# Kernel tuning notes

Hardware: AMD Instinct MI355X
Metric: run time of the kernel (lower is better)

Reference implementation:

```python
import jax, jax.numpy as jnp
import numpy as np

GRID = 2
SPAN = 2.0
EMBED = 64
HIDDEN = 128
PRED_LEN = 12
N = 1024
T = 8
SCENE_SIZE = 64


def _social_pool(ht, pos, scene, active):
    """ht: [N,H], pos: [N,2], scene: [N] int, active: [N] bool -> [N, GRID*GRID, H].
    Vectorized equivalent of the per-scene scatter_add pooling: pairwise mask over
    same-scene, active, within-area, non-self pairs; bin neighbor hidden states."""
    n = ht.shape[0]
    half = SPAN / 2.0
    eps = 0.01
    rel = pos[None, :, :] - pos[:, None, :]  # rel[i,j] = pos_j - pos_i
    within = ((rel[..., 0] < half - eps) & (rel[..., 0] > -half + eps)
              & (rel[..., 1] < half - eps) & (rel[..., 1] > -half + eps))
    pair = (within & (~jnp.eye(n, dtype=bool))
            & (scene[:, None] == scene[None, :])
            & active[:, None] & active[None, :])
    cell = SPAN / GRID
    gidx = jnp.floor((rel + half) / cell).astype(jnp.int32)
    gid = jnp.clip(gidx[..., 0] * GRID + gidx[..., 1], 0, GRID * GRID - 1)
    onehot = jax.nn.one_hot(gid, GRID * GRID, dtype=ht.dtype) * pair[..., None].astype(ht.dtype)
    # pooled[i,g,h] = sum_j onehot[i,j,g] * ht[j,h]
    return jnp.einsum('ijg,jh->igh', onehot, ht)


def _lstm_step(x, h, c, Wih, Whh, bih, bhh):
    z = x @ Wih.T + bih + h @ Whh.T + bhh
    i, f, g, o = jnp.split(z, 4, axis=-1)
    c_new = jax.nn.sigmoid(f) * c + jax.nn.sigmoid(i) * jnp.tanh(g)
    h_new = jax.nn.sigmoid(o) * jnp.tanh(c_new)
    return h_new, c_new


def setup_inputs() -> dict:
    key = jax.random.key(0)
    ks = jax.random.split(key, 16)
    past_traj = jax.random.uniform(ks[0], (N, T, 2), dtype=jnp.float32) * 8.0
    past_traj_rel = jax.random.normal(ks[1], (N, T, 2), dtype=jnp.float32)
    past_traj_timestamp_mask = jnp.ones((N, T), dtype=jnp.int32)
    is_predictable = jnp.ones((N, 1), dtype=jnp.int32)
    same_scene_mask = (jnp.arange(N, dtype=jnp.int32) // SCENE_SIZE).reshape(N, 1)

    def lin(k, fan_out, fan_in):
        b = 1.0 / np.sqrt(fan_in)
        return jax.random.uniform(k, (fan_out, fan_in), jnp.float32, -b, b)

    pos_W = lin(ks[2], EMBED, 2)
    pos_b = jnp.zeros((EMBED,), jnp.float32)
    soc_W = lin(ks[3], EMBED, GRID * GRID * HIDDEN)
    soc_b = jnp.zeros((EMBED,), jnp.float32)
    Wih = lin(ks[4], 4 * HIDDEN, 2 * EMBED)
    Whh = lin(ks[5], 4 * HIDDEN, HIDDEN)
    bih = jnp.zeros((4 * HIDDEN,), jnp.float32)
    bhh = jnp.zeros((4 * HIDDEN,), jnp.float32)
    h0 = jax.random.normal(ks[6], (HIDDEN,), jnp.float32) * 0.1
    c0 = jax.random.normal(ks[7], (HIDDEN,), jnp.float32) * 0.1
    pred_W = lin(ks[8], 5, HIDDEN)
    pred_b = jnp.zeros((5,), jnp.float32)
    return {
        'past_traj': past_traj, 'past_traj_rel': past_traj_rel,
        'past_traj_timestamp_mask': past_traj_timestamp_mask,
        'is_predictable': is_predictable, 'same_scene_mask': same_scene_mask,
        'pos_W': pos_W, 'pos_b': pos_b, 'soc_W': soc_W, 'soc_b': soc_b,
        'Wih': Wih, 'Whh': Whh, 'bih': bih, 'bhh': bhh,
        'h0': h0, 'c0': c0, 'pred_W': pred_W, 'pred_b': pred_b,
    }


def reference(past_traj, past_traj_rel, past_traj_timestamp_mask, is_predictable,
              same_scene_mask, pos_W, pos_b, soc_W, soc_b, Wih, Whh, bih, bhh,
              h0, c0, pred_W, pred_b):
    n = past_traj.shape[0]
    scene = same_scene_mask[:, 0]
    ht = jnp.broadcast_to(h0[None, :], (n, HIDDEN))
    ct = jnp.broadcast_to(c0[None, :], (n, HIDDEN))

    def obs_step(carry, inp):
        ht, ct = carry
        point, rel, m = inp  # [N,2], [N,2], [N]
        active = m == 1
        pooled = _social_pool(ht, point, scene, active)  # [N,G^2,H]
        et = jax.nn.relu(rel @ pos_W.T + pos_b)
        at = jax.nn.relu(pooled.reshape(n, -1) @ soc_W.T + soc_b)
        x = jnp.concatenate([et, at], axis=-1)
        h_new, c_new = _lstm_step(x, ht, ct, Wih, Whh, bih, bhh)
        ht = jnp.where(active[:, None], h_new, ht)
        ct = jnp.where(active[:, None], c_new, ct)
        return (ht, ct), None

    obs_inp = (jnp.moveaxis(past_traj, 1, 0), jnp.moveaxis(past_traj_rel, 1, 0),
               jnp.moveaxis(past_traj_timestamp_mask, 1, 0))
    (ht, ct), _ = jax.lax.scan(obs_step, (ht, ct), obs_inp)

    pred_active = past_traj_timestamp_mask[:, -1] == 1
    pos0 = past_traj[:, -1, :]

    def pred_step(carry, _):
        ht, ct, pos = carry
        out = ht @ pred_W.T + pred_b  # [N,5]
        rel = out[:, :2]
        pos = pos + rel
        pooled = _social_pool(ht, pos, scene, pred_active)
        et = jax.nn.relu(rel @ pos_W.T + pos_b)
        at = jax.nn.relu(pooled.reshape(n, -1) @ soc_W.T + soc_b)
        x = jnp.concatenate([et, at], axis=-1)
        h_new, c_new = _lstm_step(x, ht, ct, Wih, Whh, bih, bhh)
        ht = jnp.where(pred_active[:, None], h_new, ht)
        ct = jnp.where(pred_active[:, None], c_new, ct)
        return (ht, ct, pos), (out, pos)

    (_, _, _), (outs, trajs) = jax.lax.scan(pred_step, (ht, ct, pos0), None, length=PRED_LEN)
    pred_out_all = jnp.where(pred_active[:, None, None], jnp.moveaxis(outs, 0, 1), 0.0)
    pred_traj_all = jnp.where(pred_active[:, None, None], jnp.moveaxis(trajs, 0, 1), 0.0)
    # is_predictable is all-ones in this setup, so the final boolean filter is identity
    return pred_out_all, pred_traj_all
```

## Files before the change

kernel.cpp:

```cpp
#include <hip/hip_runtime.h>

#define NAGENT 64
#define HID    128
#define TOBS   8
#define PREDL  12
#define NTHR   1024
#define XH     136
#define PP     264
#define SPP    268

typedef __attribute__((ext_vector_type(8))) short bf16x8;
typedef __attribute__((ext_vector_type(4))) short bf16x4;
typedef __attribute__((ext_vector_type(4))) float f32x4;
typedef __attribute__((ext_vector_type(4))) int   i32x4;
typedef __attribute__((ext_vector_type(2))) unsigned int u32x2;

__device__ __forceinline__ unsigned short f2bf(float f) {
    unsigned int x = __float_as_uint(f);
    unsigned int r = (x + 0x7fffu + ((x >> 16) & 1u)) >> 16;
    return (unsigned short)r;
}
__device__ __forceinline__ float bf2f(unsigned short u) {
    return __uint_as_float(((unsigned int)u) << 16);
}
__device__ __forceinline__ float sigmf(float x) {
    return __builtin_amdgcn_rcpf(1.0f + __expf(-x));
}
__device__ __forceinline__ float tanhf_fast(float x) {
    x = fminf(fmaxf(x, -15.0f), 15.0f);
    float e = __expf(2.0f * x);
    return (e - 1.0f) * __builtin_amdgcn_rcpf(e + 1.0f);
}
__device__ __forceinline__ float sel4(float a0, float a1, float a2, float a3, int k) {
    float lo = (k & 1) ? a1 : a0;
    float hi = (k & 1) ? a3 : a2;
    return (k & 2) ? hi : lo;
}

__global__ void prep_weights(const float* __restrict__ Wih, const float* __restrict__ Whh,
                             const float* __restrict__ socW, const float* __restrict__ predW,
                             unsigned short* __restrict__ wd, unsigned short* __restrict__ wb,
                             unsigned short* __restrict__ wp) {
    int idx = blockIdx.x * 256 + threadIdx.x;
    if (idx < 131072) {
        int e = idx & 7, l = (idx >> 3) & 63, t = idx >> 9;
        int kt = t & 7, nt = t >> 3;
        int k = kt * 32 + ((l >> 4) << 3) + e;
        int n = nt * 16 + (l & 15);
        int d = n >> 2, g = n & 3;
        int row = g * 128 + d;
        float v = (k < 128) ? Wih[row * 128 + k] : Whh[row * 128 + (k - 128)];
        wd[idx] = f2bf(v);
    } else if (idx < 163840) {
        int i2 = idx - 131072;
        int e = i2 & 7, l = (i2 >> 3) & 63, t = i2 >> 9;
        int kt = t & 3, nt = t >> 2;
        int k = kt * 32 + ((l >> 4) << 3) + e;
        int r = nt * 16 + (l & 15);
        int eo = r >> 2, g = r & 3;
        wb[i2] = f2bf(socW[eo * 512 + g * 128 + k]);
    } else if (idx < 167936) {
        int i3 = idx - 163840;
        int e = i3 & 7, l = (i3 >> 3) & 63, f = i3 >> 9;
        int kt = f & 3, half = f >> 2;
        int k = kt * 32 + ((l >> 4) << 3) + e;
        int n = l & 15;
        float v = (n < 5) ? predW[n * 128 + k] : 0.0f;
        unsigned short hi = f2bf(v);
        wp[i3] = half ? f2bf(v - bf2f(hi)) : hi;
    }
}

__global__ __launch_bounds__(NTHR) void social_lstm_mfma(
    const float* __restrict__ past_traj, const float* __restrict__ past_traj_rel,
    const int* __restrict__ ts_mask, const int* __restrict__ scene_in,
    const float* __restrict__ pos_W, const float* __restrict__ pos_b,
    const float* __restrict__ soc_b,
    const float* __restrict__ bih, const float* __restrict__ bhh,
    const float* __restrict__ h0, const float* __restrict__ c0,
    const float* __restrict__ pred_b,
    const unsigned short* __restrict__ wd, const unsigned short* __restrict__ wb,
    const unsigned short* __restrict__ wp,
    float* __restrict__ out)
{
    __shared__ __align__(16) unsigned short sh_X[NAGENT][XH];
    __shared__ __align__(16) unsigned short sh_H[2][NAGENT][XH];
    __shared__ __align__(16) unsigned short sh_P[NAGENT][PP];
    __shared__ __align__(16) unsigned short sh_S[NAGENT][SPP];
    __shared__ float sh_px[2][NAGENT], sh_py[2][NAGENT];
    __shared__ float sh_rx[2][NAGENT], sh_ry[2][NAGENT];
    __shared__ __align__(16) int sh_act[2][NAGENT];
    __shared__ int sh_scene[NAGENT];

    const int tid  = threadIdx.x;
    const int lane = tid & 63;
    const int wv   = __builtin_amdgcn_readfirstlane(tid >> 6);
    const int gbase = blockIdx.x * NAGENT;
    const int c16 = lane & 15;
    const int q4  = lane >> 4;
    const int go  = c16 & 3;
    const int dq  = c16 >> 2;

    float bs[2], c_st[4][2];
    int dimv[2];
    #pragma unroll
    for (int s = 0; s < 2; ++s) {
        const int n = (2 * wv + s) * 16 + c16;
        const int d = n >> 2, g = n & 3;
        bs[s] = bih[g * 128 + d] + bhh[g * 128 + d];
        dimv[s] = (2 * wv + s) * 4 + dq;
        #pragma unroll
        for (int mj = 0; mj < 4; ++mj) c_st[mj][s] = c0[dimv[s]];
    }
    for (int p = tid; p < NAGENT * HID; p += NTHR) {
        int a = p >> 7, d = p & 127;
        sh_H[0][a][d] = f2bf(h0[d]);
    }
    if (tid < NAGENT) {
        const int ig = gbase + tid;
        sh_scene[tid] = scene_in[ig];
        sh_px[0][tid] = past_traj[(ig * TOBS + 0) * 2 + 0];
        sh_py[0][tid] = past_traj[(ig * TOBS + 0) * 2 + 1];
        sh_rx[0][tid] = past_traj_rel[(ig * TOBS + 0) * 2 + 0];
        sh_ry[0][tid] = past_traj_rel[(ig * TOBS + 0) * 2 + 1];
        sh_act[0][tid] = (ts_mask[ig * TOBS + 0] == 1) ? 1 : 0;
    }
    __syncthreads();

    const bf16x8* wdp = (const bf16x8*)wd + (2 * wv * 8) * 64 + lane;
    const bf16x8* wbp = (const bf16x8*)wb + (wv * 4) * 64 + lane;

    for (int step = 0; step < TOBS + PREDL; ++step) {
        const int pb = step & 1;
        const int hb = step & 1;
        const int ab = (step < TOBS) ? pb : 1;

        if (step >= TOBS) {
            if (wv < 4) {
                const bf16x8* wpv = (const bf16x8*)wp;
                f32x4 pa = (f32x4){0.f, 0.f, 0.f, 0.f};
                #pragma unroll
                for (int kt = 0; kt < 4; ++kt) {
                    const bf16x8 a = *(const bf16x8*)&sh_H[hb][wv * 16 + c16][kt * 32 + q4 * 8];
                    pa = __builtin_amdgcn_mfma_f32_16x16x32_bf16(a, wpv[kt * 64 + lane], pa, 0, 0, 0);
                    pa = __builtin_amdgcn_mfma_f32_16x16x32_bf16(a, wpv[(4 + kt) * 64 + lane], pa, 0, 0, 0);
                }
                if (c16 < 5) {
                    const float pbias = pred_b[c16];
                    const int p = step - TOBS;
                    const int pprev = (step - 1) & 1;
                    #pragma unroll
                    for (int rr = 0; rr < 4; ++rr) {
                        const int a = wv * 16 + q4 * 4 + rr;
                        const float o = pa[rr] + pbias;
                        const float m = sh_act[1][a] ? 1.0f : 0.0f;
                        const int ig = gbase + a;
                        out[(ig * PREDL + p) * 5 + c16] = m * o;
                        if (c16 == 0) {
                            const float px = sh_px[pprev][a] + o;
                            sh_px[pb][a] = px; sh_rx[pb][a] = o;
                            out[61440 + (ig * PREDL + p) * 2 + 0] = m * px;
                        }
                        if (c16 == 1) {
                            const float py = sh_py[pprev][a] + o;
                            sh_py[pb][a] = py; sh_ry[pb][a] = o;
                            out[61440 + (ig * PREDL + p) * 2 + 1] = m * py;
                        }
                    }
                }
            }
            __syncthreads();
        }

        #pragma unroll
        for (int it = 0; it < 4; ++it) {
            const int p = it * NTHR + tid;
            const int i = p >> 6, j = p & 63;
            const float dx = sh_px[pb][j] - sh_px[pb][i];
            const float dy = sh_py[pb][j] - sh_py[pb][i];
            const bool within = (dx < 0.99f) & (dx > -0.99f) & (dy < 0.99f) & (dy > -0.99f);
            const bool pair = within && (i != j) && (sh_scene[i] == sh_scene[j])
                              && sh_act[ab][i] && sh_act[ab][j];
            const int gid = ((dx >= 0.f) ? 2 : 0) + ((dy >= 0.f) ? 1 : 0);
            unsigned int w0 = 0, w1 = 0;
            if (pair) {
                if (gid == 0) w0 = 0x3f80u;
                else if (gid == 1) w0 = 0x3f800000u;
                else if (gid == 2) w1 = 0x3f80u;
                else w1 = 0x3f800000u;
            }
            u32x2 w; w[0] = w0; w[1] = w1;
            *(u32x2*)&sh_P[i][j * 4] = w;
        }
        {
            const float rx = sh_rx[pb][lane], ry = sh_ry[pb][lane];
            const int e0 = wv * 4;
            #pragma unroll
            for (int u = 0; u < 4; ++u) {
                const int e = e0 + u;
                sh_X[lane][e] = f2bf(fmaxf(pos_b[e] + rx * pos_W[e * 2] + ry * pos_W[e * 2 + 1], 0.f));
            }
        }
        {
            f32x4 acc2[4];
            #pragma unroll
            for (int mj = 0; mj < 4; ++mj) acc2[mj] = (f32x4){0.f, 0.f, 0.f, 0.f};
            #pragma unroll
            for (int kt = 0; kt < 4; ++kt) {
                const bf16x8 b = wbp[kt * 64];
                #pragma unroll
                for (int mj = 0; mj < 4; ++mj) {
                    const bf16x8 a = *(const bf16x8*)&sh_H[hb][mj * 16 + c16][kt * 32 + q4 * 8];
                    acc2[mj] = __builtin_amdgcn_mfma_f32_16x16x32_bf16(a, b, acc2[mj], 0, 0, 0);
                }
            }
            const int rcol = wv * 16 + c16;
            #pragma unroll
            for (int mj = 0; mj < 4; ++mj)
                #pragma unroll
                for (int rr = 0; rr < 4; ++rr)
                    sh_S[mj * 16 + q4 * 4 + rr][rcol] = f2bf(acc2[mj][rr]);
        }
        __syncthreads();

        {
            const int mt = wv & 3, nt = wv >> 2;
            const int cb = 4 * (nt * 16 + c16);
            f32x4 cac = (f32x4){0.f, 0.f, 0.f, 0.f};
            #pragma unroll
            for (int kt = 0; kt < 8; ++kt) {
                const bf16x8 a = *(const bf16x8*)&sh_P[mt * 16 + c16][kt * 32 + q4 * 8];
                const int j0 = kt * 8 + q4 * 2;
                const bf16x4 lo = *(const bf16x4*)&sh_S[j0][cb];
                const bf16x4 hi = *(const bf16x4*)&sh_S[j0 + 1][cb];
                const bf16x8 b = __builtin_shufflevector(lo, hi, 0, 1, 2, 3, 4, 5, 6, 7);
                cac = __builtin_amdgcn_mfma_f32_16x16x32_bf16(a, b, cac, 0, 0, 0);
            }
            const int e = nt * 16 + c16;
            const float sb = soc_b[e];
            #pragma unroll
            for (int rr = 0; rr < 4; ++rr)
                sh_X[mt * 16 + q4 * 4 + rr][64 + e] = f2bf(fmaxf(cac[rr] + sb, 0.f));
        }
        __syncthreads();

        {
            f32x4 acc[4][2];
            #pragma unroll
            for (int mj = 0; mj < 4; ++mj) {
                acc[mj][0] = (f32x4){0.f, 0.f, 0.f, 0.f};
                acc[mj][1] = (f32x4){0.f, 0.f, 0.f, 0.f};
            }
            #pragma unroll 2
            for (int kt = 0; kt < 8; ++kt) {
                const bf16x8 b0 = wdp[kt * 64];
                const bf16x8 b1 = wdp[kt * 64 + 512];
                #pragma unroll
                for (int mj = 0; mj < 4; ++mj) {
                    const bf16x8 a = (kt < 4)
                        ? *(const bf16x8*)&sh_X[mj * 16 + c16][kt * 32 + q4 * 8]
                        : *(const bf16x8*)&sh_H[hb][mj * 16 + c16][(kt - 4) * 32 + q4 * 8];
                    acc[mj][0] = __builtin_amdgcn_mfma_f32_16x16x32_bf16(a, b0, acc[mj][0], 0, 0, 0);
                    acc[mj][1] = __builtin_amdgcn_mfma_f32_16x16x32_bf16(a, b1, acc[mj][1], 0, 0, 0);
                }
            }
            #pragma unroll
            for (int mj = 0; mj < 4; ++mj) {
                const int a = mj * 16 + q4 * 4 + go;
                const bool act = sh_act[ab][a] != 0;
                #pragma unroll
                for (int s = 0; s < 2; ++s) {
                    const float z0 = acc[mj][s][0] + bs[s];
                    const float z1 = acc[mj][s][1] + bs[s];
                    const float z2 = acc[mj][s][2] + bs[s];
                    const float z3 = acc[mj][s][3] + bs[s];
                    const float s0 = sel4(z0, z1, z2, z3, go);
                    const float s1 = sel4(z0, z1, z2, z3, go ^ 1);
                    const float s2 = sel4(z0, z1, z2, z3, go ^ 2);
                    const float s3 = sel4(z0, z1, z2, z3, go ^ 3);
                    const float t1 = __shfl_xor(s1, 1, 64);
                    const float t2 = __shfl_xor(s2, 2, 64);
                    const float t3 = __shfl_xor(s3, 3, 64);
                    const float zi = sel4(s0, t1, t2, t3, go);
                    const float zf = sel4(s0, t1, t2, t3, go ^ 1);
                    const float zg = sel4(s0, t1, t2, t3, go ^ 2);
                    const float zo = sel4(s0, t1, t2, t3, go ^ 3);
                    const float cold = c_st[mj][s];
                    const float cn = sigmf(zf) * cold + sigmf(zi) * tanhf_fast(zg);
                    const float hn = sigmf(zo) * tanhf_fast(cn);
                    c_st[mj][s] = act ? cn : cold;
                    const float hold = bf2f(sh_H[hb][a][dimv[s]]);
                    sh_H[hb ^ 1][a][dimv[s]] = f2bf(act ? hn : hold);
                }
            }
        }
        if (step + 1 < TOBS && tid < NAGENT) {
            const int ig = gbase + tid;
            const int np = (step + 1) & 1;
            sh_px[np][tid] = past_traj[(ig * TOBS + step + 1) * 2 + 0];
            sh_py[np][tid] = past_traj[(ig * TOBS + step + 1) * 2 + 1];
            sh_rx[np][tid] = past_traj_rel[(ig * TOBS + step + 1) * 2 + 0];
            sh_ry[np][tid] = past_traj_rel[(ig * TOBS + step + 1) * 2 + 1];
            sh_act[np][tid] = (ts_mask[ig * TOBS + step + 1] == 1) ? 1 : 0;
        }
        __syncthreads();
    }
}

extern "C" void kernel_launch(void* const* d_in, const int* in_sizes, int n_in,
                              void* d_out, int out_size, void* d_ws, size_t ws_size,
                              hipStream_t stream) {
    (void)in_sizes; (void)n_in; (void)out_size; (void)ws_size;
    unsigned short* wd = (unsigned short*)d_ws;
    unsigned short* wb = wd + 131072;
    unsigned short* wp = wb + 32768;
    prep_weights<<<656, 256, 0, stream>>>(
        (const float*)d_in[9], (const float*)d_in[10],
        (const float*)d_in[7], (const float*)d_in[15], wd, wb, wp);
    social_lstm_mfma<<<16, NTHR, 0, stream>>>(
        (const float*)d_in[0],
        (const float*)d_in[1],
        (const int*)  d_in[2],
        (const int*)  d_in[4],
        (const float*)d_in[5],
        (const float*)d_in[6],
        (const float*)d_in[8],
        (const float*)d_in[11],
        (const float*)d_in[12],
        (const float*)d_in[13],
        (const float*)d_in[14],
        (const float*)d_in[16],
        wd, wb, wp,
        (float*)d_out);
}
```

Measured before the change: 299.0 us.

## Retile LSTM gate GEMM so each lane owns all four gates per dimension

Reorders the packed LSTM weights to the natural gate-major row order. Each wave now computes all four gates (i,f,g,o) for 16 hidden dims across 2 agent tiles, instead of interleaved gate columns. This removes the cross-lane shuffles and select chains in the cell update and keeps h in registers rather than rereading the old h from LDS. The social GEMM is retiled to 2x2 tiles per wave with the same goal of reusing A and B operands, which raises per-wave B-fragment global loads and register pressure.

```diff
diff --git a/kernel.cpp b/kernel.cpp
--- a/kernel.cpp
+++ b/kernel.cpp
@@ -30,11 +30,6 @@
     x = fminf(fmaxf(x, -15.0f), 15.0f);
     float e = __expf(2.0f * x);
     return (e - 1.0f) * __builtin_amdgcn_rcpf(e + 1.0f);
-}
-__device__ __forceinline__ float sel4(float a0, float a1, float a2, float a3, int k) {
-    float lo = (k & 1) ? a1 : a0;
-    float hi = (k & 1) ? a3 : a2;
-    return (k & 2) ? hi : lo;
 }
 
 __global__ void prep_weights(const float* __restrict__ Wih, const float* __restrict__ Whh,
@@ -47,9 +42,7 @@
         int kt = t & 7, nt = t >> 3;
         int k = kt * 32 + ((l >> 4) << 3) + e;
         int n = nt * 16 + (l & 15);
-        int d = n >> 2, g = n & 3;
-        int row = g * 128 + d;
-        float v = (k < 128) ? Wih[row * 128 + k] : Whh[row * 128 + (k - 128)];
+        float v = (k < 128) ? Wih[n * 128 + k] : Whh[n * 128 + (k - 128)];
         wd[idx] = f2bf(v);
     } else if (idx < 163840) {
         int i2 = idx - 131072;
@@ -98,19 +91,22 @@
     const int gbase = blockIdx.x * NAGENT;
     const int c16 = lane & 15;
     const int q4  = lane >> 4;
-    const int go  = c16 & 3;
-    const int dq  = c16 >> 2;
-
-    float bs[2], c_st[4][2];
-    int dimv[2];
-    #pragma unroll
-    for (int s = 0; s < 2; ++s) {
-        const int n = (2 * wv + s) * 16 + c16;
-        const int d = n >> 2, g = n & 3;
-        bs[s] = bih[g * 128 + d] + bhh[g * 128 + d];
-        dimv[s] = (2 * wv + s) * 4 + dq;
+
+    const int sub8 = wv & 7;
+    const int mjg  = wv >> 3;
+    const int dim  = sub8 * 16 + c16;
+
+    const float bs0 = bih[0 * 128 + dim] + bhh[0 * 128 + dim];
+    const float bs1 = bih[1 * 128 + dim] + bhh[1 * 128 + dim];
+    const float bs2 = bih[2 * 128 + dim] + bhh[2 * 128 + dim];
+    const float bs3 = bih[3 * 128 + dim] + bhh[3 * 128 + dim];
+    float c_st[2][4], h_rg[2][4];
+    {
+        const float cz = c0[dim], hz = h0[dim];
         #pragma unroll
-        for (int mj = 0; mj < 4; ++mj) c_st[mj][s] = c0[dimv[s]];
+        for (int m = 0; m < 2; ++m)
+            #pragma unroll
+            for (int r = 0; r < 4; ++r) { c_st[m][r] = cz; h_rg[m][r] = hz; }
     }
     for (int p = tid; p < NAGENT * HID; p += NTHR) {
         int a = p >> 7, d = p & 127;
@@ -127,8 +123,8 @@
     }
     __syncthreads();
 
-    const bf16x8* wdp = (const bf16x8*)wd + (2 * wv * 8) * 64 + lane;
-    const bf16x8* wbp = (const bf16x8*)wb + (wv * 4) * 64 + lane;
+    const bf16x8* wdv = (const bf16x8*)wd;
+    const bf16x8* wbv = (const bf16x8*)wb;
 
     for (int step = 0; step < TOBS + PREDL; ++step) {
         const int pb = step & 1;
@@ -202,24 +198,29 @@
             }
         }
         {
-            f32x4 acc2[4];
-            #pragma unroll
-            for (int mj = 0; mj < 4; ++mj) acc2[mj] = (f32x4){0.f, 0.f, 0.f, 0.f};
+            f32x4 bac[2][2];
+            bac[0][0] = (f32x4){0,0,0,0}; bac[0][1] = (f32x4){0,0,0,0};
+            bac[1][0] = (f32x4){0,0,0,0}; bac[1][1] = (f32x4){0,0,0,0};
             #pragma unroll
             for (int kt = 0; kt < 4; ++kt) {
-                const bf16x8 b = wbp[kt * 64];
-                #pragma unroll
-                for (int mj = 0; mj < 4; ++mj) {
-                    const bf16x8 a = *(const bf16x8*)&sh_H[hb][mj * 16 + c16][kt * 32 + q4 * 8];
-                    acc2[mj] = __builtin_amdgcn_mfma_f32_16x16x32_bf16(a, b, acc2[mj], 0, 0, 0);
-                }
-            }
-            const int rcol = wv * 16 + c16;
-            #pragma unroll
-            for (int mj = 0; mj < 4; ++mj)
-                #pragma unroll
-                for (int rr = 0; rr < 4; ++rr)
-                    sh_S[mj * 16 + q4 * 4 + rr][rcol] = f2bf(acc2[mj][rr]);
+                const bf16x8 a0 = *(const bf16x8*)&sh_H[hb][(2 * mjg + 0) * 16 + c16][kt * 32 + q4 * 8];
+                const bf16x8 a1 = *(const bf16x8*)&sh_H[hb][(2 * mjg + 1) * 16 + c16][kt * 32 + q4 * 8];
+                const bf16x8 b0 = wbv[((2 * sub8 + 0) * 4 + kt) * 64 + lane];
+                const bf16x8 b1 = wbv[((2 * sub8 + 1) * 4 + kt) * 64 + lane];
+                bac[0][0] = __builtin_amdgcn_mfma_f32_16x16x32_bf16(a0, b0, bac[0][0], 0, 0, 0);
+                bac[0][1] = __builtin_amdgcn_mfma_f32_16x16x32_bf16(a0, b1, bac[0][1], 0, 0, 0);
+                bac[1][0] = __builtin_amdgcn_mfma_f32_16x16x32_bf16(a1, b0, bac[1][0], 0, 0, 0);
+                bac[1][1] = __builtin_amdgcn_mfma_f32_16x16x32_bf16(a1, b1, bac[1][1], 0, 0, 0);
+            }
+            #pragma unroll
+            for (int mjl = 0; mjl < 2; ++mjl)
+                #pragma unroll
+                for (int s = 0; s < 2; ++s) {
+                    const int rcol = (2 * sub8 + s) * 16 + c16;
+                    #pragma unroll
+                    for (int rr = 0; rr < 4; ++rr)
+                        sh_S[(2 * mjg + mjl) * 16 + q4 * 4 + rr][rcol] = f2bf(bac[mjl][s][rr]);
+                }
         }
         __syncthreads();
 
@@ -245,52 +246,42 @@
         __syncthreads();
 
         {
-            f32x4 acc[4][2];
-            #pragma unroll
-            for (int mj = 0; mj < 4; ++mj) {
-                acc[mj][0] = (f32x4){0.f, 0.f, 0.f, 0.f};
-                acc[mj][1] = (f32x4){0.f, 0.f, 0.f, 0.f};
-            }
+            f32x4 acc[2][4];
+            #pragma unroll
+            for (int m = 0; m < 2; ++m)
+                #pragma unroll
+                for (int g = 0; g < 4; ++g) acc[m][g] = (f32x4){0.f, 0.f, 0.f, 0.f};
             #pragma unroll 2
             for (int kt = 0; kt < 8; ++kt) {
-                const bf16x8 b0 = wdp[kt * 64];
-                const bf16x8 b1 = wdp[kt * 64 + 512];
-                #pragma unroll
-                for (int mj = 0; mj < 4; ++mj) {
-                    const bf16x8 a = (kt < 4)
-                        ? *(const bf16x8*)&sh_X[mj * 16 + c16][kt * 32 + q4 * 8]
-                        : *(const bf16x8*)&sh_H[hb][mj * 16 + c16][(kt - 4) * 32 + q4 * 8];
-                    acc[mj][0] = __builtin_amdgcn_mfma_f32_16x16x32_bf16(a, b0, acc[mj][0], 0, 0, 0);
-                    acc[mj][1] = __builtin_amdgcn_mfma_f32_16x16x32_bf16(a, b1, acc[mj][1], 0, 0, 0);
-                }
-            }
-            #pragma unroll
-            for (int mj = 0; mj < 4; ++mj) {
-                const int a = mj * 16 + q4 * 4 + go;
-                const bool act = sh_act[ab][a] != 0;
-                #pragma unroll
-                for (int s = 0; s < 2; ++s) {
-                    const float z0 = acc[mj][s][0] + bs[s];
-                    const float z1 = acc[mj][s][1] + bs[s];
-                    const float z2 = acc[mj][s][2] + bs[s];
-                    const float z3 = acc[mj][s][3] + bs[s];
-                    const float s0 = sel4(z0, z1, z2, z3, go);
-                    const float s1 = sel4(z0, z1, z2, z3, go ^ 1);
-                    const float s2 = sel4(z0, z1, z2, z3, go ^ 2);
-                    const float s3 = sel4(z0, z1, z2, z3, go ^ 3);
-                    const float t1 = __shfl_xor(s1, 1, 64);
-                    const float t2 = __shfl_xor(s2, 2, 64);
-                    const float t3 = __shfl_xor(s3, 3, 64);
-                    const float zi = sel4(s0, t1, t2, t3, go);
-                    const float zf = sel4(s0, t1, t2, t3, go ^ 1);
-                    const float zg = sel4(s0, t1, t2, t3, go ^ 2);
-                    const float zo = sel4(s0, t1, t2, t3, go ^ 3);
-                    const float cold = c_st[mj][s];
+                const bf16x8 a0 = (kt < 4)
+                    ? *(const bf16x8*)&sh_X[(2 * mjg + 0) * 16 + c16][kt * 32 + q4 * 8]
+                    : *(const bf16x8*)&sh_H[hb][(2 * mjg + 0) * 16 + c16][(kt - 4) * 32 + q4 * 8];
+                const bf16x8 a1 = (kt < 4)
+                    ? *(const bf16x8*)&sh_X[(2 * mjg + 1) * 16 + c16][kt * 32 + q4 * 8]
+                    : *(const bf16x8*)&sh_H[hb][(2 * mjg + 1) * 16 + c16][(kt - 4) * 32 + q4 * 8];
+                #pragma unroll
+                for (int g = 0; g < 4; ++g) {
+                    const bf16x8 b = wdv[((g * 8 + sub8) * 8 + kt) * 64 + lane];
+                    acc[0][g] = __builtin_amdgcn_mfma_f32_16x16x32_bf16(a0, b, acc[0][g], 0, 0, 0);
+                    acc[1][g] = __builtin_amdgcn_mfma_f32_16x16x32_bf16(a1, b, acc[1][g], 0, 0, 0);
+                }
+            }
+            #pragma unroll
+            for (int mjl = 0; mjl < 2; ++mjl) {
+                const i32x4 a4 = *(const i32x4*)&sh_act[ab][(2 * mjg + mjl) * 16 + q4 * 4];
+                #pragma unroll
+                for (int rr = 0; rr < 4; ++rr) {
+                    const float zi = acc[mjl][0][rr] + bs0;
+                    const float zf = acc[mjl][1][rr] + bs1;
+                    const float zg = acc[mjl][2][rr] + bs2;
+                    const float zo = acc[mjl][3][rr] + bs3;
+                    const float cold = c_st[mjl][rr];
                     const float cn = sigmf(zf) * cold + sigmf(zi) * tanhf_fast(zg);
                     const float hn = sigmf(zo) * tanhf_fast(cn);
-                    c_st[mj][s] = act ? cn : cold;
-                    const float hold = bf2f(sh_H[hb][a][dimv[s]]);
-                    sh_H[hb ^ 1][a][dimv[s]] = f2bf(act ? hn : hold);
+                    const bool act = a4[rr] != 0;
+                    c_st[mjl][rr] = act ? cn : cold;
+                    h_rg[mjl][rr] = act ? hn : h_rg[mjl][rr];
+                    sh_H[hb ^ 1][(2 * mjg + mjl) * 16 + q4 * 4 + rr][dim] = f2bf(h_rg[mjl][rr]);
                 }
             }
         }
```

Result: slower. 308.6 us (+3.2%).
